# Optimization experiments

Measured on AMD Instinct MI355X. Metric: run time of the kernel, lower is better.

## Reference

```python
import jax, jax.numpy as jnp
import numpy as np

NEG_SLOPE = 0.2


def gatv2_conv(h, src, dst, W, attn, n_nodes, residual=False, W_res=None, activation=None):
    """DGL GATv2Conv with share_weights=True, bias=False, no dropout (eval).

    h: [N, F_in]; W: [F_in, H*D]; attn: [H, D]; src/dst: [E] edge endpoints.
    Returns [N, H, D].
    """
    H, D = attn.shape
    feat = (h @ W).reshape(n_nodes, H, D)              # shared src/dst projection
    # GATv2 scoring: e_ij = a^T LeakyReLU(W h_i + W h_j)
    e = jax.nn.leaky_relu(feat[src] + feat[dst], NEG_SLOPE)   # [E, H, D]
    logits = jnp.einsum('ehd,hd->eh', e, attn)                 # [E, H]
    # edge softmax over incoming edges of each dst node
    m = jax.ops.segment_max(logits, dst, num_segments=n_nodes)  # [N, H]
    ex = jnp.exp(logits - jax.lax.stop_gradient(m)[dst])
    denom = jax.ops.segment_sum(ex, dst, num_segments=n_nodes)  # [N, H]
    a = ex / denom[dst]                                          # [E, H]
    # aggregate: sum_j a_ij * (W h_j)
    rst = jax.ops.segment_sum(a[:, :, None] * feat[src], dst, num_segments=n_nodes)  # [N, H, D]
    if residual:
        res = h @ W_res if W_res is not None else h
        rst = rst + res.reshape(n_nodes, H, D)
    if activation is not None:
        rst = activation(rst)
    return rst


def setup_inputs() -> dict:
    key = jax.random.key(0)
    ks = jax.random.split(key, 12)
    N, E, F_IN, D, H, C, HO = 50000, 500000, 128, 32, 4, 40, 6
    inputs = jax.random.normal(ks[0], (N, F_IN), dtype=jnp.float32)
    src = jax.random.randint(ks[1], (E,), 0, N)
    dst = jax.random.randint(ks[2], (E,), 0, N)
    def glorot(k, shape):
        fan = shape[0]
        return jax.random.normal(k, shape, dtype=jnp.float32) / np.sqrt(fan)
    W0 = glorot(ks[3], (F_IN, H * D))
    attn0 = glorot(ks[4], (H, D))
    W1 = glorot(ks[5], (H * D, H * D))
    attn1 = glorot(ks[6], (H, D))
    W2 = glorot(ks[7], (H * D, HO * C))
    attn2 = glorot(ks[8], (HO, C))
    Wres2 = glorot(ks[9], (H * D, HO * C))
    return {"inputs": inputs, "src": src, "dst": dst, "W0": W0, "attn0": attn0,
            "W1": W1, "attn1": attn1, "W2": W2, "attn2": attn2, "Wres2": Wres2}


def reference(inputs, src, dst, W0, attn0, W1, attn1, W2, attn2, Wres2):
    N = inputs.shape[0]
    act = jax.nn.elu
    # layer 0: no residual, elu, flatten heads
    h = gatv2_conv(inputs, src, dst, W0, attn0, N, residual=False, activation=act)
    h = h.reshape(N, -1)
    # layer 1: identity residual (in == heads*out), elu, flatten heads
    h = gatv2_conv(h, src, dst, W1, attn1, N, residual=True, W_res=None, activation=act)
    h = h.reshape(N, -1)
    # output layer: linear residual, no activation, mean over heads
    out = gatv2_conv(h, src, dst, W2, attn2, N, residual=True, W_res=Wres2, activation=None)
    return out.mean(axis=1)  # [N, num_classes]
```

## Files before the change

kernel.cpp:

```cpp
#include <hip/hip_runtime.h>
#include <math.h>


#define LRELU(x) ((x) >= 0.f ? (x) : 0.2f * (x))

__global__ void k_zero(int* __restrict__ cnt, int* __restrict__ fill, int N) {
  int i = blockIdx.x * blockDim.x + threadIdx.x;
  if (i < N) { cnt[i] = 0; fill[i] = 0; }
}

__global__ void k_count(const int* __restrict__ dst, int* __restrict__ cnt, int E) {
  int e = blockIdx.x * blockDim.x + threadIdx.x;
  if (e < E) atomicAdd(&cnt[dst[e]], 1);
}

__global__ void k_scan1(const int* __restrict__ cnt, int* __restrict__ row_ptr,
                        int* __restrict__ bsum, int N) {
  __shared__ int s[256];
  int tid = threadIdx.x;
  int i = blockIdx.x * 256 + tid;
  int v = (i < N) ? cnt[i] : 0;
  s[tid] = v;
  __syncthreads();
  for (int off = 1; off < 256; off <<= 1) {
    int t = (tid >= off) ? s[tid - off] : 0;
    __syncthreads();
    s[tid] += t;
    __syncthreads();
  }
  if (i < N) row_ptr[i] = s[tid] - v;
  if (tid == 255) bsum[blockIdx.x] = s[255];
}

__global__ void k_scan2(int* __restrict__ bsum, int nb) {
  __shared__ int s[256];
  int t = threadIdx.x;
  int v = (t < nb) ? bsum[t] : 0;
  s[t] = v;
  __syncthreads();
  for (int off = 1; off < 256; off <<= 1) {
    int tt = (t >= off) ? s[t - off] : 0;
    __syncthreads();
    s[t] += tt;
    __syncthreads();
  }
  if (t < nb) bsum[t] = s[t] - v;
}

__global__ void k_scan3(int* __restrict__ row_ptr, const int* __restrict__ bsum, int N, int E) {
  int i = blockIdx.x * blockDim.x + threadIdx.x;
  if (i < N) row_ptr[i] += bsum[i >> 8];
  else if (i == N) row_ptr[N] = E;
}

__global__ void k_scatter(const int* __restrict__ src, const int* __restrict__ dst,
                          const int* __restrict__ row_ptr, int* __restrict__ fill,
                          int* __restrict__ csr_src, int E) {
  int e = blockIdx.x * blockDim.x + threadIdx.x;
  if (e >= E) return;
  int d = dst[e];
  int pos = row_ptr[d] + atomicAdd(&fill[d], 1);
  csr_src[pos] = src[e];
}

__global__ void k_wmean(const float* __restrict__ wres2, float* __restrict__ wm) {
  int i = blockIdx.x * blockDim.x + threadIdx.x;
  if (i >= 128 * 40) return;
  int k = i / 40, c = i % 40;
  float s = 0.f;
#pragma unroll
  for (int ho = 0; ho < 6; ++ho) s += wres2[k * 240 + ho * 40 + c];
  wm[i] = s * (1.0f / 6.0f);
}

template <int LDC>
__global__ __launch_bounds__(256) void k_gemm(const float* __restrict__ A,
                                              const float* __restrict__ B,
                                              float* __restrict__ C, int N) {
  __shared__ __align__(16) float As[32][64];
  __shared__ __align__(16) float Bs[32][128];
  const int tid = threadIdx.x;
  const int row0 = blockIdx.x * 64;
  const int col_base = (blockIdx.y == 0) ? 0 : (LDC - 128);
  const int ty = tid >> 4, tx = tid & 15;
  const int r0 = ty * 4;
  const int arow = tid & 63;
  const int akc = (tid >> 6) * 8;
  int gra = row0 + arow;
  if (gra >= N) gra = N - 1;
  const float* Ap = A + (size_t)gra * 128 + akc;
  const int f0 = tid * 4;
  const int br0 = f0 >> 7, bc0 = f0 & 127;

  float acc[4][8] = {};

#pragma unroll 1
  for (int kk = 0; kk < 128; kk += 32) {
    __syncthreads();
    float4 a0 = *(const float4*)(Ap + kk);
    float4 a1 = *(const float4*)(Ap + kk + 4);
    float4 bv0 = *(const float4*)&B[(size_t)(kk + br0 + 0) * LDC + col_base + bc0];
    float4 bv1 = *(const float4*)&B[(size_t)(kk + br0 + 8) * LDC + col_base + bc0];
    float4 bv2 = *(const float4*)&B[(size_t)(kk + br0 + 16) * LDC + col_base + bc0];
    float4 bv3 = *(const float4*)&B[(size_t)(kk + br0 + 24) * LDC + col_base + bc0];
    As[akc + 0][arow] = a0.x;
    As[akc + 1][arow] = a0.y;
    As[akc + 2][arow] = a0.z;
    As[akc + 3][arow] = a0.w;
    As[akc + 4][arow] = a1.x;
    As[akc + 5][arow] = a1.y;
    As[akc + 6][arow] = a1.z;
    As[akc + 7][arow] = a1.w;
    *(float4*)&Bs[br0 + 0][bc0] = bv0;
    *(float4*)&Bs[br0 + 8][bc0] = bv1;
    *(float4*)&Bs[br0 + 16][bc0] = bv2;
    *(float4*)&Bs[br0 + 24][bc0] = bv3;
    __syncthreads();
#pragma unroll
    for (int k = 0; k < 32; ++k) {
      float a[4], b[8];
      *(float4*)&a[0] = *(const float4*)&As[k][r0];
      *(float4*)&b[0] = *(const float4*)&Bs[k][tx * 4];
      *(float4*)&b[4] = *(const float4*)&Bs[k][64 + tx * 4];
#pragma unroll
      for (int ii = 0; ii < 4; ++ii)
#pragma unroll
        for (int jj = 0; jj < 8; ++jj) acc[ii][jj] += a[ii] * b[jj];
    }
  }

  const int gc_lo = col_base + tx * 4;
  const int gc_hi = col_base + 64 + tx * 4;
  const bool lo_ok = (blockIdx.y == 0) || (gc_lo >= 128);
#pragma unroll
  for (int i = 0; i < 4; ++i) {
    int gr = row0 + r0 + i;
    if (gr < N) {
      if (lo_ok) *(float4*)&C[(size_t)gr * LDC + gc_lo] = *(float4*)&acc[i][0];
      *(float4*)&C[(size_t)gr * LDC + gc_hi] = *(float4*)&acc[i][4];
    }
  }
}

__global__ __launch_bounds__(256) void k_resmean(const float* __restrict__ A,
                                                 const float* __restrict__ Wm,
                                                 float* __restrict__ out, int N) {
  __shared__ float w[128 * 40];
  for (int i = threadIdx.x; i < 128 * 40; i += 256) w[i] = Wm[i];
  __syncthreads();
  int r = blockIdx.x * 256 + threadIdx.x;
  if (r >= N) return;
  float acc[40] = {};
  for (int k = 0; k < 128; k += 4) {
    float4 hv = *(const float4*)&A[(size_t)r * 128 + k];
#pragma unroll
    for (int j = 0; j < 40; ++j)
      acc[j] += hv.x * w[(k + 0) * 40 + j] + hv.y * w[(k + 1) * 40 + j] +
                hv.z * w[(k + 2) * 40 + j] + hv.w * w[(k + 3) * 40 + j];
  }
#pragma unroll
  for (int j = 0; j < 40; j += 4)
    *(float4*)&out[(size_t)r * 40 + j] = make_float4(acc[j], acc[j + 1], acc[j + 2], acc[j + 3]);
}

template <bool RES>
__global__ __launch_bounds__(256) void k_agg_fused(const float* __restrict__ feat,
                                                   const float* __restrict__ attn,
                                                   const int* __restrict__ row_ptr,
                                                   const int* __restrict__ csr_src,
                                                   const float* __restrict__ hres,
                                                   float* __restrict__ out, int N) {
  int wid = (blockIdx.x * 256 + threadIdx.x) >> 6;
  bool nok = wid < N;
  int n = nok ? wid : (N - 1);
  int lane = threadIdx.x & 63;
  int half = lane >> 5;
  int c = (lane & 31) * 4;
  float4 fd = *(const float4*)&feat[(size_t)n * 128 + c];
  float4 av = *(const float4*)&attn[c];
  int p0 = row_ptr[n], p1 = row_ptr[n + 1];
  float4 zero = {0.f, 0.f, 0.f, 0.f};
  float sA = 0.f, sB = 0.f;
  float4 aA = zero, aB = zero;
  for (int p = p0; p < p1; p += 4) {
    int pA = p + half;
    int pB = p + 2 + half;
    bool vA = pA < p1, vB = pB < p1;
    int iA = csr_src[vA ? pA : p0];
    int iB = csr_src[vB ? pB : p0];
    float4 fA = *(const float4*)&feat[(size_t)iA * 128 + c];
    float4 fB = *(const float4*)&feat[(size_t)iB * 128 + c];
    float xA = av.x * LRELU(fA.x + fd.x) + av.y * LRELU(fA.y + fd.y) +
               av.z * LRELU(fA.z + fd.z) + av.w * LRELU(fA.w + fd.w);
    float xB = av.x * LRELU(fB.x + fd.x) + av.y * LRELU(fB.y + fd.y) +
               av.z * LRELU(fB.z + fd.z) + av.w * LRELU(fB.w + fd.w);
    xA += __shfl_xor(xA, 1);
    xB += __shfl_xor(xB, 1);
    xA += __shfl_xor(xA, 2);
    xB += __shfl_xor(xB, 2);
    xA += __shfl_xor(xA, 4);
    xB += __shfl_xor(xB, 4);
    float peA = vA ? __expf(xA) : 0.f;
    float peB = vB ? __expf(xB) : 0.f;
    sA += peA;
    aA.x += peA * fA.x;
    aA.y += peA * fA.y;
    aA.z += peA * fA.z;
    aA.w += peA * fA.w;
    sB += peB;
    aB.x += peB * fB.x;
    aB.y += peB * fB.y;
    aB.z += peB * fB.z;
    aB.w += peB * fB.w;
  }
  sA += sB;
  aA.x += aB.x; aA.y += aB.y; aA.z += aB.z; aA.w += aB.w;
  float s2 = __shfl_xor(sA, 32);
  float4 a2;
  a2.x = __shfl_xor(aA.x, 32);
  a2.y = __shfl_xor(aA.y, 32);
  a2.z = __shfl_xor(aA.z, 32);
  a2.w = __shfl_xor(aA.w, 32);
  float ssum = sA + s2;
  float inv = (p1 > p0) ? 1.0f / ssum : 0.f;
  float4 r;
  r.x = (aA.x + a2.x) * inv;
  r.y = (aA.y + a2.y) * inv;
  r.z = (aA.z + a2.z) * inv;
  r.w = (aA.w + a2.w) * inv;
  if (RES) {
    float4 hv = *(const float4*)&hres[(size_t)n * 128 + c];
    r.x += hv.x; r.y += hv.y; r.z += hv.z; r.w += hv.w;
  }
  r.x = r.x > 0.f ? r.x : expm1f(r.x);
  r.y = r.y > 0.f ? r.y : expm1f(r.y);
  r.z = r.z > 0.f ? r.z : expm1f(r.z);
  r.w = r.w > 0.f ? r.w : expm1f(r.w);
  if (half == 0 && nok) *(float4*)&out[(size_t)n * 128 + c] = r;
}

__global__ __launch_bounds__(256) void k_agg2_fused(const float* __restrict__ feat2,
                                                    const float* __restrict__ attn2,
                                                    const int* __restrict__ row_ptr,
                                                    const int* __restrict__ csr_src,
                                                    const float* __restrict__ resm,
                                                    float* __restrict__ out, int N) {
  __shared__ float rs[4][240];
  int w = threadIdx.x >> 6;
  int wid = blockIdx.x * 4 + w;
  bool nok = wid < N;
  int n = nok ? wid : (N - 1);
  int lane = threadIdx.x & 63;
  bool act = lane < 60;
  int ho = lane / 10, t = lane % 10;
  int g0 = ho * 10;
  int fo = act ? (ho * 40 + t * 4) : 0;
  float4 zero = {0.f, 0.f, 0.f, 0.f};
  float4 fd = act ? *(const float4*)&feat2[(size_t)n * 240 + fo] : zero;
  float4 av = act ? *(const float4*)&attn2[fo] : zero;
  int p0 = row_ptr[n], p1 = row_ptr[n + 1];
  float s_[4];
  float4 a_[4];
#pragma unroll
  for (int j = 0; j < 4; ++j) { s_[j] = 0.f; a_[j] = zero; }
  for (int p = p0; p < p1; p += 4) {
    int idx[4];
    bool val[4];
#pragma unroll
    for (int j = 0; j < 4; ++j) {
      int pp = p + j;
      val[j] = pp < p1;
      idx[j] = csr_src[val[j] ? pp : p];
    }
    float4 f_[4];
#pragma unroll
    for (int j = 0; j < 4; ++j) f_[j] = *(const float4*)&feat2[(size_t)idx[j] * 240 + fo];
    float x_[4], aa_[4], S_[4];
#pragma unroll
    for (int j = 0; j < 4; ++j)
      x_[j] = av.x * LRELU(f_[j].x + fd.x) + av.y * LRELU(f_[j].y + fd.y) +
              av.z * LRELU(f_[j].z + fd.z) + av.w * LRELU(f_[j].w + fd.w);
#pragma unroll
    for (int j = 0; j < 4; ++j) aa_[j] = x_[j] + __shfl(x_[j], lane + 5);
#pragma unroll
    for (int j = 0; j < 4; ++j) S_[j] = aa_[j] + __shfl(aa_[j], lane + 1);
#pragma unroll
    for (int j = 0; j < 4; ++j) S_[j] = S_[j] + __shfl(S_[j], lane + 2);
#pragma unroll
    for (int j = 0; j < 4; ++j) S_[j] = S_[j] + __shfl(aa_[j], lane + 4);
#pragma unroll
    for (int j = 0; j < 4; ++j) {
      float l = __shfl(S_[j], g0);
      float pe = val[j] ? __expf(l) : 0.f;
      s_[j] += pe;
      a_[j].x += pe * f_[j].x;
      a_[j].y += pe * f_[j].y;
      a_[j].z += pe * f_[j].z;
      a_[j].w += pe * f_[j].w;
    }
  }
  float ssum = (s_[0] + s_[1]) + (s_[2] + s_[3]);
  float4 at;
  at.x = (a_[0].x + a_[1].x) + (a_[2].x + a_[3].x);
  at.y = (a_[0].y + a_[1].y) + (a_[2].y + a_[3].y);
  at.z = (a_[0].z + a_[1].z) + (a_[2].z + a_[3].z);
  at.w = (a_[0].w + a_[1].w) + (a_[2].w + a_[3].w);
  float inv = (p1 > p0) ? 1.0f / ssum : 0.f;
  float4 r;
  r.x = at.x * inv;
  r.y = at.y * inv;
  r.z = at.z * inv;
  r.w = at.w * inv;
  if (act) *(float4*)&rs[w][fo] = r;
  __syncthreads();
  if (lane < 10 && nok) {
#pragma unroll
    for (int k = 0; k < 4; ++k) {
      int cc = t * 4 + k;
      float v = (rs[w][cc] + rs[w][40 + cc] + rs[w][80 + cc] + rs[w][120 + cc] +
                 rs[w][160 + cc] + rs[w][200 + cc]) * (1.0f / 6.0f) +
                resm[(size_t)n * 40 + cc];
      out[(size_t)n * 40 + cc] = v;
    }
  }
}

extern "C" void kernel_launch(void* const* d_in, const int* in_sizes, int n_in,
                              void* d_out, int out_size, void* d_ws, size_t ws_size,
                              hipStream_t stream) {
  const float* inputs = (const float*)d_in[0];
  const int* src = (const int*)d_in[1];
  const int* dst = (const int*)d_in[2];
  const float* W0 = (const float*)d_in[3];
  const float* attn0 = (const float*)d_in[4];
  const float* W1 = (const float*)d_in[5];
  const float* attn1 = (const float*)d_in[6];
  const float* W2 = (const float*)d_in[7];
  const float* attn2 = (const float*)d_in[8];
  const float* Wres2 = (const float*)d_in[9];
  const int N = in_sizes[0] / 128;
  const int E = in_sizes[1];

  char* base = (char*)d_ws;
  size_t off = 0;
  auto alloc = [&](size_t bytes) -> void* {
    void* q = base + off;
    off += (bytes + 255) & ~(size_t)255;
    return q;
  };
  int* cnt = (int*)alloc((size_t)N * 4);
  int* fill = (int*)alloc((size_t)N * 4);
  int* row_ptr = (int*)alloc((size_t)(N + 1) * 4);
  int* bsum = (int*)alloc(1024 * 4);
  int* csr_src = (int*)alloc((size_t)E * 4);
  float* F = (float*)alloc((size_t)N * 240 * 4);
  float* h1 = (float*)alloc((size_t)N * 128 * 4);
  float* h2 = (float*)alloc((size_t)N * 128 * 4);
  float* resm = (float*)alloc((size_t)N * 40 * 4);
  float* wm = (float*)alloc(128 * 40 * 4);
  (void)ws_size;

  const int nb1 = (N + 255) / 256;
  const int nrb = (N + 63) / 64;

  hipLaunchKernelGGL(k_zero, dim3((N + 255) / 256), dim3(256), 0, stream, cnt, fill, N);
  hipLaunchKernelGGL(k_count, dim3((E + 255) / 256), dim3(256), 0, stream, dst, cnt, E);
  hipLaunchKernelGGL(k_scan1, dim3(nb1), dim3(256), 0, stream, cnt, row_ptr, bsum, N);
  hipLaunchKernelGGL(k_scan2, dim3(1), dim3(256), 0, stream, bsum, nb1);
  hipLaunchKernelGGL(k_scan3, dim3((N + 256) / 256), dim3(256), 0, stream, row_ptr, bsum, N, E);
  hipLaunchKernelGGL(k_scatter, dim3((E + 255) / 256), dim3(256), 0, stream, src, dst, row_ptr,
                     fill, csr_src, E);
  hipLaunchKernelGGL(k_wmean, dim3((128 * 40 + 255) / 256), dim3(256), 0, stream, Wres2, wm);

  hipLaunchKernelGGL((k_gemm<128>), dim3(nrb, 1), dim3(256), 0, stream, inputs, W0, F, N);
  hipLaunchKernelGGL((k_agg_fused<false>), dim3((N + 3) / 4), dim3(256), 0, stream, F, attn0,
                     row_ptr, csr_src, (const float*)nullptr, h1, N);
  hipLaunchKernelGGL((k_gemm<128>), dim3(nrb, 1), dim3(256), 0, stream, h1, W1, F, N);
  hipLaunchKernelGGL((k_agg_fused<true>), dim3((N + 3) / 4), dim3(256), 0, stream, F, attn1,
                     row_ptr, csr_src, h1, h2, N);
  hipLaunchKernelGGL((k_gemm<240>), dim3(nrb, 2), dim3(256), 0, stream, h2, W2, F, N);
  hipLaunchKernelGGL(k_resmean, dim3((N + 255) / 256), dim3(256), 0, stream, h2, wm, resm, N);
  hipLaunchKernelGGL(k_agg2_fused, dim3((N + 3) / 4), dim3(256), 0, stream, F, attn2, row_ptr,
                     csr_src, resm, (float*)d_out, N);
}
```

Baseline: 437.4 us.

## Prefetch GEMM tiles into registers and unroll edge gathers to eight per iteration

The projection GEMM now loads the next K-tile of A and B into registers while the current tile is written to shared memory and consumed, overlapping global loads with compute. Both aggregation kernels now process eight edges per loop iteration instead of four, putting more independent feature gathers in flight to hide memory latency. The wider unrolling raises register pressure and adds more masked work when a node has few in-edges (average in-degree is about 10).

```diff
diff --git a/kernel.cpp b/kernel.cpp
--- a/kernel.cpp
+++ b/kernel.cpp
@@ -94,15 +94,16 @@
 
   float acc[4][8] = {};
 
+  float4 a0 = *(const float4*)(Ap + 0);
+  float4 a1 = *(const float4*)(Ap + 4);
+  float4 bv0 = *(const float4*)&B[(size_t)(br0 + 0) * LDC + col_base + bc0];
+  float4 bv1 = *(const float4*)&B[(size_t)(br0 + 8) * LDC + col_base + bc0];
+  float4 bv2 = *(const float4*)&B[(size_t)(br0 + 16) * LDC + col_base + bc0];
+  float4 bv3 = *(const float4*)&B[(size_t)(br0 + 24) * LDC + col_base + bc0];
+
 #pragma unroll 1
-  for (int kk = 0; kk < 128; kk += 32) {
-    __syncthreads();
-    float4 a0 = *(const float4*)(Ap + kk);
-    float4 a1 = *(const float4*)(Ap + kk + 4);
-    float4 bv0 = *(const float4*)&B[(size_t)(kk + br0 + 0) * LDC + col_base + bc0];
-    float4 bv1 = *(const float4*)&B[(size_t)(kk + br0 + 8) * LDC + col_base + bc0];
-    float4 bv2 = *(const float4*)&B[(size_t)(kk + br0 + 16) * LDC + col_base + bc0];
-    float4 bv3 = *(const float4*)&B[(size_t)(kk + br0 + 24) * LDC + col_base + bc0];
+  for (int i = 0; i < 4; ++i) {
+    __syncthreads();
     As[akc + 0][arow] = a0.x;
     As[akc + 1][arow] = a0.y;
     As[akc + 2][arow] = a0.z;
@@ -115,6 +116,15 @@
     *(float4*)&Bs[br0 + 8][bc0] = bv1;
     *(float4*)&Bs[br0 + 16][bc0] = bv2;
     *(float4*)&Bs[br0 + 24][bc0] = bv3;
+    if (i < 3) {
+      const int kk = (i + 1) * 32;
+      a0 = *(const float4*)(Ap + kk);
+      a1 = *(const float4*)(Ap + kk + 4);
+      bv0 = *(const float4*)&B[(size_t)(kk + br0 + 0) * LDC + col_base + bc0];
+      bv1 = *(const float4*)&B[(size_t)(kk + br0 + 8) * LDC + col_base + bc0];
+      bv2 = *(const float4*)&B[(size_t)(kk + br0 + 16) * LDC + col_base + bc0];
+      bv3 = *(const float4*)&B[(size_t)(kk + br0 + 24) * LDC + col_base + bc0];
+    }
     __syncthreads();
 #pragma unroll
     for (int k = 0; k < 32; ++k) {
@@ -182,36 +192,54 @@
   float4 zero = {0.f, 0.f, 0.f, 0.f};
   float sA = 0.f, sB = 0.f;
   float4 aA = zero, aB = zero;
-  for (int p = p0; p < p1; p += 4) {
-    int pA = p + half;
-    int pB = p + 2 + half;
-    bool vA = pA < p1, vB = pB < p1;
-    int iA = csr_src[vA ? pA : p0];
-    int iB = csr_src[vB ? pB : p0];
-    float4 fA = *(const float4*)&feat[(size_t)iA * 128 + c];
-    float4 fB = *(const float4*)&feat[(size_t)iB * 128 + c];
-    float xA = av.x * LRELU(fA.x + fd.x) + av.y * LRELU(fA.y + fd.y) +
-               av.z * LRELU(fA.z + fd.z) + av.w * LRELU(fA.w + fd.w);
-    float xB = av.x * LRELU(fB.x + fd.x) + av.y * LRELU(fB.y + fd.y) +
-               av.z * LRELU(fB.z + fd.z) + av.w * LRELU(fB.w + fd.w);
-    xA += __shfl_xor(xA, 1);
-    xB += __shfl_xor(xB, 1);
-    xA += __shfl_xor(xA, 2);
-    xB += __shfl_xor(xB, 2);
-    xA += __shfl_xor(xA, 4);
-    xB += __shfl_xor(xB, 4);
-    float peA = vA ? __expf(xA) : 0.f;
-    float peB = vB ? __expf(xB) : 0.f;
-    sA += peA;
-    aA.x += peA * fA.x;
-    aA.y += peA * fA.y;
-    aA.z += peA * fA.z;
-    aA.w += peA * fA.w;
-    sB += peB;
-    aB.x += peB * fB.x;
-    aB.y += peB * fB.y;
-    aB.z += peB * fB.z;
-    aB.w += peB * fB.w;
+  for (int p = p0; p < p1; p += 8) {
+    int pe_[4];
+    bool v_[4];
+    int i_[4];
+#pragma unroll
+    for (int j = 0; j < 4; ++j) {
+      pe_[j] = p + 2 * j + half;
+      v_[j] = pe_[j] < p1;
+      i_[j] = csr_src[v_[j] ? pe_[j] : p0];
+    }
+    float4 f0v = *(const float4*)&feat[(size_t)i_[0] * 128 + c];
+    float4 f1v = *(const float4*)&feat[(size_t)i_[1] * 128 + c];
+    float4 f2v = *(const float4*)&feat[(size_t)i_[2] * 128 + c];
+    float4 f3v = *(const float4*)&feat[(size_t)i_[3] * 128 + c];
+    float x0 = av.x * LRELU(f0v.x + fd.x) + av.y * LRELU(f0v.y + fd.y) +
+               av.z * LRELU(f0v.z + fd.z) + av.w * LRELU(f0v.w + fd.w);
+    float x1 = av.x * LRELU(f1v.x + fd.x) + av.y * LRELU(f1v.y + fd.y) +
+               av.z * LRELU(f1v.z + fd.z) + av.w * LRELU(f1v.w + fd.w);
+    float x2 = av.x * LRELU(f2v.x + fd.x) + av.y * LRELU(f2v.y + fd.y) +
+               av.z * LRELU(f2v.z + fd.z) + av.w * LRELU(f2v.w + fd.w);
+    float x3 = av.x * LRELU(f3v.x + fd.x) + av.y * LRELU(f3v.y + fd.y) +
+               av.z * LRELU(f3v.z + fd.z) + av.w * LRELU(f3v.w + fd.w);
+    x0 += __shfl_xor(x0, 1);
+    x1 += __shfl_xor(x1, 1);
+    x2 += __shfl_xor(x2, 1);
+    x3 += __shfl_xor(x3, 1);
+    x0 += __shfl_xor(x0, 2);
+    x1 += __shfl_xor(x1, 2);
+    x2 += __shfl_xor(x2, 2);
+    x3 += __shfl_xor(x3, 2);
+    x0 += __shfl_xor(x0, 4);
+    x1 += __shfl_xor(x1, 4);
+    x2 += __shfl_xor(x2, 4);
+    x3 += __shfl_xor(x3, 4);
+    float e0 = v_[0] ? __expf(x0) : 0.f;
+    float e1 = v_[1] ? __expf(x1) : 0.f;
+    float e2 = v_[2] ? __expf(x2) : 0.f;
+    float e3 = v_[3] ? __expf(x3) : 0.f;
+    sA += e0 + e2;
+    sB += e1 + e3;
+    aA.x += e0 * f0v.x + e2 * f2v.x;
+    aA.y += e0 * f0v.y + e2 * f2v.y;
+    aA.z += e0 * f0v.z + e2 * f2v.z;
+    aA.w += e0 * f0v.w + e2 * f2v.w;
+    aB.x += e1 * f1v.x + e3 * f3v.x;
+    aB.y += e1 * f1v.y + e3 * f3v.y;
+    aB.z += e1 * f1v.z + e3 * f3v.z;
+    aB.w += e1 * f1v.w + e3 * f3v.w;
   }
   sA += sB;
   aA.x += aB.x; aA.y += aB.y; aA.z += aB.z; aA.w += aB.w;
@@ -263,40 +291,40 @@
   float4 a_[4];
 #pragma unroll
   for (int j = 0; j < 4; ++j) { s_[j] = 0.f; a_[j] = zero; }
-  for (int p = p0; p < p1; p += 4) {
-    int idx[4];
-    bool val[4];
-#pragma unroll
-    for (int j = 0; j < 4; ++j) {
+  for (int p = p0; p < p1; p += 8) {
+    int idx[8];
+    bool val[8];
+#pragma unroll
+    for (int j = 0; j < 8; ++j) {
       int pp = p + j;
       val[j] = pp < p1;
       idx[j] = csr_src[val[j] ? pp : p];
     }
-    float4 f_[4];
-#pragma unroll
-    for (int j = 0; j < 4; ++j) f_[j] = *(const float4*)&feat2[(size_t)idx[j] * 240 + fo];
-    float x_[4], aa_[4], S_[4];
-#pragma unroll
-    for (int j = 0; j < 4; ++j)
+    float4 f_[8];
+#pragma unroll
+    for (int j = 0; j < 8; ++j) f_[j] = *(const float4*)&feat2[(size_t)idx[j] * 240 + fo];
+    float x_[8], aa_[8], S_[8];
+#pragma unroll
+    for (int j = 0; j < 8; ++j)
       x_[j] = av.x * LRELU(f_[j].x + fd.x) + av.y * LRELU(f_[j].y + fd.y) +
               av.z * LRELU(f_[j].z + fd.z) + av.w * LRELU(f_[j].w + fd.w);
 #pragma unroll
-    for (int j = 0; j < 4; ++j) aa_[j] = x_[j] + __shfl(x_[j], lane + 5);
-#pragma unroll
-    for (int j = 0; j < 4; ++j) S_[j] = aa_[j] + __shfl(aa_[j], lane + 1);
-#pragma unroll
-    for (int j = 0; j < 4; ++j) S_[j] = S_[j] + __shfl(S_[j], lane + 2);
-#pragma unroll
-    for (int j = 0; j < 4; ++j) S_[j] = S_[j] + __shfl(aa_[j], lane + 4);
-#pragma unroll
-    for (int j = 0; j < 4; ++j) {
+    for (int j = 0; j < 8; ++j) aa_[j] = x_[j] + __shfl(x_[j], lane + 5);
+#pragma unroll
+    for (int j = 0; j < 8; ++j) S_[j] = aa_[j] + __shfl(aa_[j], lane + 1);
+#pragma unroll
+    for (int j = 0; j < 8; ++j) S_[j] = S_[j] + __shfl(S_[j], lane + 2);
+#pragma unroll
+    for (int j = 0; j < 8; ++j) S_[j] = S_[j] + __shfl(aa_[j], lane + 4);
+#pragma unroll
+    for (int j = 0; j < 8; ++j) {
       float l = __shfl(S_[j], g0);
       float pe = val[j] ? __expf(l) : 0.f;
-      s_[j] += pe;
-      a_[j].x += pe * f_[j].x;
-      a_[j].y += pe * f_[j].y;
-      a_[j].z += pe * f_[j].z;
-      a_[j].w += pe * f_[j].w;
+      s_[j & 3] += pe;
+      a_[j & 3].x += pe * f_[j].x;
+      a_[j & 3].y += pe * f_[j].y;
+      a_[j & 3].z += pe * f_[j].z;
+      a_[j & 3].w += pe * f_[j].w;
     }
   }
   float ssum = (s_[0] + s_[1]) + (s_[2] + s_[3]);
```

Result: slower. 448.7 us (+2.6%).
